# Kernel tuning notes

Measured on AMD Instinct MI355X. Metric: run time of the kernel, lower is better.

Reference implementation:

```python
import jax, jax.numpy as jnp
import numpy as np

B, S, E, H, HD, M = 2, 2048, 1024, 16, 64, 2048  # batch, seq, embed, heads, head_dim, mem_width


def setup_inputs() -> dict:
    key = jax.random.key(0)
    k1, k2, k3, k4, k5 = jax.random.split(key, 5)
    tensor = jax.random.normal(k1, (B, S, E), dtype=jnp.float32)
    # QueryProj: Linear(E -> [H, HD]) with weight + bias (kaiming-style scale)
    Wq = jax.random.normal(k2, (E, H, HD), dtype=jnp.float32) / np.sqrt(E)
    bq = jnp.zeros((H, HD), dtype=jnp.float32)
    # Learnable key/value memory banks [H, M, HD]
    K = jax.random.normal(k3, (H, M, HD), dtype=jnp.float32) / np.sqrt(HD)
    V = jax.random.normal(k4, (H, M, HD), dtype=jnp.float32) / np.sqrt(HD)
    # DeheadProj: Linear([H, HD] -> E)
    Wd = jax.random.normal(k5, (H, HD, E), dtype=jnp.float32) / np.sqrt(H * HD)
    bd = jnp.zeros((E,), dtype=jnp.float32)
    return {"tensor": tensor, "Wq": Wq, "bq": bq, "K": K, "V": V, "Wd": Wd, "bd": bd}


def reference(tensor, Wq, bq, K, V, Wd, bd):
    # Head-splitting query projection: [B,S,E] -> [B,S,H,HD]
    q = jnp.einsum('bse,ehd->bshd', tensor, Wq) + bq
    # Attention logits against fixed parameter memory: [B,S,H,M]
    logits = jnp.einsum('bshd,hmd->bshm', q, K)
    score = jax.nn.softmax(logits, axis=-1)  # mode == 'softmax'
    # Value readout, scaled AFTER the matmul by sqrt(head_dim) (as in source)
    attn = jnp.einsum('bshm,hmd->bshd', score, V) / jnp.sqrt(jnp.asarray(HD, dtype=q.dtype))
    # Dehead projection back to embedding width: [B,S,E]
    out = jnp.einsum('bshd,hde->bse', attn, Wd) + bd
    return out
```

## Files before the change

kernel.cpp:

```cpp
#include <hip/hip_runtime.h>

typedef _Float16 half8 __attribute__((ext_vector_type(8)));
typedef _Float16 half4v __attribute__((ext_vector_type(4)));
typedef __fp16 fp16x2 __attribute__((ext_vector_type(2)));
typedef float f32x4 __attribute__((ext_vector_type(4)));
typedef float float4v __attribute__((ext_vector_type(4)));

constexpr int NS = 4096;
constexpr int E  = 1024;
constexpr int H  = 16;
constexpr int HD = 64;
constexpr int M  = 2048;
constexpr int HE = 1024;

__device__ __forceinline__ void gload16(const _Float16* g, _Float16* l) {
  __builtin_amdgcn_global_load_lds((__attribute__((address_space(1))) void*)g,
                                   (__attribute__((address_space(3))) void*)l, 16, 0, 0);
}

__device__ __forceinline__ float fexp2(float x) {
#if __has_builtin(__builtin_amdgcn_exp2f)
  return __builtin_amdgcn_exp2f(x);
#else
  return __expf(x * 0.6931471805599453f);
#endif
}


__global__ void cvt_f32_to_f16(const float* __restrict__ in, _Float16* __restrict__ out,
                               float scale) {
  int i = (blockIdx.x * 256 + threadIdx.x) * 4;
  float4v v = *(const float4v*)(in + i);
  half4v o = { (_Float16)(v[0] * scale), (_Float16)(v[1] * scale),
               (_Float16)(v[2] * scale), (_Float16)(v[3] * scale) };
  *(half4v*)(out + i) = o;
}

__global__ void transpose_cvt(const float* __restrict__ in, _Float16* __restrict__ out,
                              int R, int C) {
  __shared__ float tile[32][33];
  int b = blockIdx.z;
  in  += (size_t)b * R * C;
  out += (size_t)b * R * C;
  int c0 = blockIdx.x * 32, r0 = blockIdx.y * 32;
  int tx = threadIdx.x, ty = threadIdx.y;
#pragma unroll
  for (int i = 0; i < 4; ++i)
    tile[ty + 8 * i][tx] = in[(size_t)(r0 + ty + 8 * i) * C + c0 + tx];
  __syncthreads();
#pragma unroll
  for (int i = 0; i < 4; ++i)
    out[(size_t)(c0 + ty + 8 * i) * R + r0 + tx] = (_Float16)tile[tx][ty + 8 * i];
}

__global__ void transpose_cvt2(const float* __restrict__ inA, const float* __restrict__ inB,
                               _Float16* __restrict__ outA, _Float16* __restrict__ outB) {
  __shared__ float tile[32][33];
  const float* in = blockIdx.z ? inB : inA;
  _Float16* out = blockIdx.z ? outB : outA;
  int c0 = blockIdx.x * 32, r0 = blockIdx.y * 32;
  int tx = threadIdx.x, ty = threadIdx.y;
#pragma unroll
  for (int i = 0; i < 4; ++i)
    tile[ty + 8 * i][tx] = in[(size_t)(r0 + ty + 8 * i) * 1024 + c0 + tx];
  __syncthreads();
#pragma unroll
  for (int i = 0; i < 4; ++i)
    out[(size_t)(c0 + ty + 8 * i) * 1024 + r0 + tx] = (_Float16)tile[tx][ty + 8 * i];
}


template <typename OUT_T>
__global__ __launch_bounds__(512, 4) void gemm_f16(
    const _Float16* __restrict__ A,
    const _Float16* __restrict__ Bt,
    const float* __restrict__ bias,
    OUT_T* __restrict__ C,
    int Ncols, int K, float scale)
{
  __shared__ alignas(16) _Float16 Ab[2][8 * 512];
  __shared__ alignas(16) _Float16 Bb[2][4 * 512];
  const int tid = threadIdx.x;
  const int wave = tid >> 6, lane = tid & 63;
  const int l15 = lane & 15, l4 = lane >> 4;

  const int nwg = gridDim.x;
  int wg = (blockIdx.x & 7) * (nwg >> 3) + (blockIdx.x >> 3);
  const int nbn = Ncols >> 6;
  const int mblk = wg / nbn, nblk = wg % nbn;

  const _Float16* aS = A  + (size_t)(mblk * 128 + wave * 16 + l15) * K + l4 * 8;
  const _Float16* bS = Bt + (size_t)(nblk * 64 + (wave & 3) * 16 + l15) * K + l4 * 8;
  _Float16* aD0 = &Ab[0][wave * 512];
  _Float16* aD1 = &Ab[1][wave * 512];
  _Float16* bD0 = &Bb[0][(wave & 3) * 512];
  _Float16* bD1 = &Bb[1][(wave & 3) * 512];

  const int wr = wave >> 1, wc = wave & 1;
  f32x4 acc[2][2];
#pragma unroll
  for (int i = 0; i < 2; ++i)
#pragma unroll
    for (int n = 0; n < 2; ++n) acc[i][n] = (f32x4){0.f, 0.f, 0.f, 0.f};

  gload16(aS, aD0);
  if (wave < 4) gload16(bS, bD0);
  aS += 32; bS += 32;

  const int nk = K >> 5;
  for (int kt = 0; kt < nk; ++kt) {
    if (kt + 1 < nk) {
      gload16(aS, (kt & 1) ? aD0 : aD1);
      if (wave < 4) gload16(bS, (kt & 1) ? bD0 : bD1);
      aS += 32; bS += 32;
      if (wave < 4) { asm volatile("s_waitcnt vmcnt(2)" ::: "memory"); }
      else          { asm volatile("s_waitcnt vmcnt(1)" ::: "memory"); }
    } else {
      asm volatile("s_waitcnt vmcnt(0)" ::: "memory");
    }
    __builtin_amdgcn_s_barrier();
    const _Float16* Ac = (kt & 1) ? &Ab[1][0] : &Ab[0][0];
    const _Float16* Bc = (kt & 1) ? &Bb[1][0] : &Bb[0][0];
    half8 af[2], bf[2];
#pragma unroll
    for (int i = 0; i < 2; ++i) af[i] = *(const half8*)(Ac + (wr * 2 + i) * 512 + lane * 8);
#pragma unroll
    for (int n = 0; n < 2; ++n) bf[n] = *(const half8*)(Bc + (wc * 2 + n) * 512 + lane * 8);
    __builtin_amdgcn_s_setprio(1);
#pragma unroll
    for (int i = 0; i < 2; ++i)
#pragma unroll
      for (int n = 0; n < 2; ++n)
        acc[i][n] = __builtin_amdgcn_mfma_f32_16x16x32_f16(af[i], bf[n], acc[i][n], 0, 0, 0);
    __builtin_amdgcn_s_setprio(0);
    asm volatile("s_waitcnt lgkmcnt(0)" ::: "memory");
    __builtin_amdgcn_sched_barrier(0);
    __builtin_amdgcn_s_barrier();
  }

  const int row0 = mblk * 128 + wr * 32;
  const int col0 = nblk * 64 + wc * 32;
#pragma unroll
  for (int n = 0; n < 2; ++n) {
    int col = col0 + n * 16 + l15;
    float bv = bias[col];
#pragma unroll
    for (int i = 0; i < 2; ++i)
#pragma unroll
      for (int r = 0; r < 4; ++r) {
        int row = row0 + i * 16 + l4 * 4 + r;
        C[(size_t)row * Ncols + col] = (OUT_T)(acc[i][n][r] * scale + bv);
      }
  }
}


__global__ __launch_bounds__(256, 4) void attn_fused(
    const _Float16* __restrict__ qh,
    const _Float16* __restrict__ Kh,
    const _Float16* __restrict__ Vth,
    _Float16* __restrict__ Op0,
    _Float16* __restrict__ Op1,
    float* __restrict__ Spart)
{
  __shared__ alignas(16) _Float16 Kb[2][4096];
  __shared__ alignas(16) _Float16 Vb[2][4096];
  __shared__ alignas(16) _Float16 Pl[4096];

  int wg = (blockIdx.x & 7) * 128 + (blockIdx.x >> 3);
  const int h = wg >> 6, half = (wg >> 5) & 1, sblk = wg & 31;
  const int m0 = half * 1024;
  const int tid = threadIdx.x;
  const int wave = tid >> 6, lane = tid & 63, l15 = lane & 15, l4 = lane >> 4;
  const int s0 = sblk * 128 + wave * 32;

  half8 qf[2][2];
#pragma unroll
  for (int f = 0; f < 2; ++f) {
    const _Float16* qp = qh + (size_t)(s0 + f * 16 + l15) * HE + h * HD + l4 * 8;
    qf[f][0] = *(const half8*)qp;
    qf[f][1] = *(const half8*)(qp + 32);
  }

  const _Float16* kSrc = Kh + (size_t)h * M * HD
                         + (size_t)((wave >> 1) * 16 + l15) * HD + (wave & 1) * 32 + l4 * 8;
  const _Float16* vSrc = Vth + (size_t)h * HD * M + (size_t)(wave * 16 + l15) * M + l4 * 8;
  const int dOff = wave * 512 + lane * 8;

  _Float16* Pw = &Pl[wave * 1024];
  const int pAddr = (l4 >> 1) * 128 + l15 * 8 + (l4 & 1) * 4;

  half8 vones;
#pragma unroll
  for (int j = 0; j < 8; ++j) vones[j] = (_Float16)1.0f;

  f32x4 acc[2][4];
  f32x4 accs[2];
#pragma unroll
  for (int f = 0; f < 2; ++f) {
    accs[f] = (f32x4){0.f, 0.f, 0.f, 0.f};
#pragma unroll
    for (int n = 0; n < 4; ++n) acc[f][n] = (f32x4){0.f, 0.f, 0.f, 0.f};
  }

#define STAGE(b, mm) {                                          \
    gload16(kSrc + (size_t)(mm) * HD,        &Kb[b][dOff]);     \
    gload16(kSrc + (size_t)((mm) + 32) * HD, &Kb[b][dOff + 2048]); \
    gload16(vSrc + (mm),                     &Vb[b][dOff]);     \
    gload16(vSrc + (mm) + 32,                &Vb[b][dOff + 2048]); }

#define CHALF(b, hh) {                                                                     \
    const _Float16* Kc = &Kb[b][(hh) * 2048];                                              \
    const _Float16* Vc = &Vb[b][(hh) * 2048];                                              \
    half8 kf[4], vf[4];                                                                    \
    _Pragma("unroll")                                                                      \
    for (int c = 0; c < 4; ++c) {                                                          \
      kf[c] = *(const half8*)(Kc + c * 512 + lane * 8);                                    \
      vf[c] = *(const half8*)(Vc + c * 512 + lane * 8);                                    \
    }                                                                                      \
    f32x4 z = (f32x4){0.f, 0.f, 0.f, 0.f};                                                 \
    f32x4 s[2][2];                                                                         \
    __builtin_amdgcn_s_setprio(1);                                                         \
    _Pragma("unroll")                                                                      \
    for (int f = 0; f < 2; ++f)                                                            \
      _Pragma("unroll")                                                                    \
      for (int t = 0; t < 2; ++t) {                                                        \
        s[f][t] = __builtin_amdgcn_mfma_f32_16x16x32_f16(kf[t * 2 + 0], qf[f][0], z, 0, 0, 0); \
        s[f][t] = __builtin_amdgcn_mfma_f32_16x16x32_f16(kf[t * 2 + 1], qf[f][1], s[f][t], 0, 0, 0); \
      }                                                                                    \
    __builtin_amdgcn_s_setprio(0);                                                         \
    _Pragma("unroll")                                                                      \
    for (int f = 0; f < 2; ++f)                                                            \
      _Pragma("unroll")                                                                    \
      for (int t = 0; t < 2; ++t) {                                                        \
        fp16x2 lo = __builtin_amdgcn_cvt_pkrtz(fexp2(s[f][t][0]), fexp2(s[f][t][1]));      \
        fp16x2 hi = __builtin_amdgcn_cvt_pkrtz(fexp2(s[f][t][2]), fexp2(s[f][t][3]));      \
        *(fp16x2*)(Pw + pAddr + f * 512 + t * 256)     = lo;                               \
        *(fp16x2*)(Pw + pAddr + f * 512 + t * 256 + 2) = hi;                               \
      }                                                                                    \
    asm volatile("s_waitcnt lgkmcnt(0)" ::: "memory");                                     \
    __builtin_amdgcn_sched_barrier(0);                                                     \
    half8 pf0 = *(const half8*)(Pw + lane * 8);                                            \
    half8 pf1 = *(const half8*)(Pw + 512 + lane * 8);                                      \
    __builtin_amdgcn_s_setprio(1);                                                         \
    _Pragma("unroll")                                                                      \
    for (int n = 0; n < 4; ++n) {                                                          \
      acc[0][n] = __builtin_amdgcn_mfma_f32_16x16x32_f16(pf0, vf[n], acc[0][n], 0, 0, 0);  \
      acc[1][n] = __builtin_amdgcn_mfma_f32_16x16x32_f16(pf1, vf[n], acc[1][n], 0, 0, 0);  \
    }                                                                                      \
    accs[0] = __builtin_amdgcn_mfma_f32_16x16x32_f16(pf0, vones, accs[0], 0, 0, 0);        \
    accs[1] = __builtin_amdgcn_mfma_f32_16x16x32_f16(pf1, vones, accs[1], 0, 0, 0);        \
    __builtin_amdgcn_s_setprio(0);                                                         \
  }

  STAGE(0, m0);
  for (int kt = 0; kt < 16; ++kt) {
    const int cur = kt & 1;
    if (kt < 15) {
      STAGE(cur ^ 1, m0 + (kt + 1) * 64);
      asm volatile("s_waitcnt vmcnt(4)" ::: "memory");
    } else {
      asm volatile("s_waitcnt vmcnt(0)" ::: "memory");
    }
    __builtin_amdgcn_s_barrier();
    CHALF(cur, 0);
    CHALF(cur, 1);
    __builtin_amdgcn_s_barrier();
  }

  _Float16* Op = half ? Op1 : Op0;
  float* Sp = Spart + (size_t)half * (NS * H);
#pragma unroll
  for (int f = 0; f < 2; ++f) {
#pragma unroll
    for (int n = 0; n < 4; ++n)
#pragma unroll
      for (int r = 0; r < 4; ++r) {
        int row = s0 + f * 16 + l4 * 4 + r;
        Op[(size_t)row * HE + h * HD + n * 16 + l15] = (_Float16)acc[f][n][r];
      }
    if (l15 == 0) {
#pragma unroll
      for (int r = 0; r < 4; ++r) {
        int row = s0 + f * 16 + l4 * 4 + r;
        Sp[(size_t)row * H + h] = accs[f][r];
      }
    }
  }
#undef STAGE
#undef CHALF
}

__global__ void attn_combine(const _Float16* __restrict__ O0, const _Float16* __restrict__ O1,
                             const float* __restrict__ Spart, _Float16* __restrict__ out) {
  int idx = (blockIdx.x * 256 + threadIdx.x) * 8;
  int row = idx >> 10, he = idx & 1023, h = he >> 6;
  half8 a = *(const half8*)(O0 + idx);
  half8 b = *(const half8*)(O1 + idx);
  float s = Spart[(size_t)row * H + h] + Spart[(size_t)(NS + row) * H + h];
  float inv = 1.0f / s;
  half8 o;
#pragma unroll
  for (int j = 0; j < 8; ++j) o[j] = (_Float16)(((float)a[j] + (float)b[j]) * inv);
  *(half8*)(out + idx) = o;
}


extern "C" void kernel_launch(void* const* d_in, const int* in_sizes, int n_in,
                              void* d_out, int out_size, void* d_ws, size_t ws_size,
                              hipStream_t stream) {
  const float* tensor = (const float*)d_in[0];
  const float* Wq     = (const float*)d_in[1];
  const float* bq     = (const float*)d_in[2];
  const float* Kp     = (const float*)d_in[3];
  const float* Vp     = (const float*)d_in[4];
  const float* Wd     = (const float*)d_in[5];
  const float* bd     = (const float*)d_in[6];
  float* out = (float*)d_out;

  char* ws = (char*)d_ws;
  _Float16* th    = (_Float16*)(ws);
  _Float16* qhb   = (_Float16*)(ws + (8  << 20));
  _Float16* attnh = (_Float16*)(ws + (16 << 20));
  _Float16* Wqt   = (_Float16*)(ws + (24 << 20));
  _Float16* Wdt   = (_Float16*)(ws + (26 << 20));
  _Float16* Khb   = (_Float16*)(ws + (28 << 20));
  _Float16* Vth   = (_Float16*)(ws + (32 << 20));
  _Float16* Op0   = (_Float16*)(ws);
  _Float16* Op1   = (_Float16*)(ws + (36 << 20));
  float*    Spart = (float*)(ws + (24 << 20));

  cvt_f32_to_f16<<<(NS * E) / 1024, 256, 0, stream>>>(tensor, th, 1.0f);
  cvt_f32_to_f16<<<(H * M * HD) / 1024, 256, 0, stream>>>(Kp, Khb, 1.44269504088896f);
  transpose_cvt2<<<dim3(32, 32, 2), dim3(32, 8), 0, stream>>>(Wq, Wd, Wqt, Wdt);
  transpose_cvt<<<dim3(2, 64, 16), dim3(32, 8), 0, stream>>>(Vp, Vth, 2048, 64);

  gemm_f16<_Float16><<<512, 512, 0, stream>>>(th, Wqt, bq, qhb, HE, E, 1.0f);
  attn_fused<<<1024, 256, 0, stream>>>(qhb, Khb, Vth, Op0, Op1, Spart);
  attn_combine<<<(NS * HE) / 2048, 256, 0, stream>>>(Op0, Op1, Spart, attnh);
  gemm_f16<float><<<512, 512, 0, stream>>>(attnh, Wdt, bd, out, E, HE, 0.125f);
}
```

Before: 120.9 us.

## Software-pipeline PV matmul one tile behind QK and exp in attention loop

After: 130.2 us. 7.6% more time.

```diff
diff --git a/kernel.cpp b/kernel.cpp
--- a/kernel.cpp
+++ b/kernel.cpp
@@ -155,7 +155,7 @@
 }
 
 
-__global__ __launch_bounds__(256, 4) void attn_fused(
+__global__ __launch_bounds__(256, 3) void attn_fused(
     const _Float16* __restrict__ qh,
     const _Float16* __restrict__ Kh,
     const _Float16* __restrict__ Vth,
@@ -203,55 +203,66 @@
     for (int n = 0; n < 4; ++n) acc[f][n] = (f32x4){0.f, 0.f, 0.f, 0.f};
   }
 
-#define STAGE(b, mm) {                                          \
-    gload16(kSrc + (size_t)(mm) * HD,        &Kb[b][dOff]);     \
+  half8 pfp[2][2];
+  half8 vfp[2][4];
+  f32x4 s[2][2];
+
+#define STAGE(b, mm) {                                             \
+    gload16(kSrc + (size_t)(mm) * HD,        &Kb[b][dOff]);        \
     gload16(kSrc + (size_t)((mm) + 32) * HD, &Kb[b][dOff + 2048]); \
-    gload16(vSrc + (mm),                     &Vb[b][dOff]);     \
+    gload16(vSrc + (mm),                     &Vb[b][dOff]);        \
     gload16(vSrc + (mm) + 32,                &Vb[b][dOff + 2048]); }
 
-#define CHALF(b, hh) {                                                                     \
-    const _Float16* Kc = &Kb[b][(hh) * 2048];                                              \
-    const _Float16* Vc = &Vb[b][(hh) * 2048];                                              \
-    half8 kf[4], vf[4];                                                                    \
-    _Pragma("unroll")                                                                      \
-    for (int c = 0; c < 4; ++c) {                                                          \
-      kf[c] = *(const half8*)(Kc + c * 512 + lane * 8);                                    \
-      vf[c] = *(const half8*)(Vc + c * 512 + lane * 8);                                    \
-    }                                                                                      \
-    f32x4 z = (f32x4){0.f, 0.f, 0.f, 0.f};                                                 \
-    f32x4 s[2][2];                                                                         \
-    __builtin_amdgcn_s_setprio(1);                                                         \
-    _Pragma("unroll")                                                                      \
-    for (int f = 0; f < 2; ++f)                                                            \
-      _Pragma("unroll")                                                                    \
-      for (int t = 0; t < 2; ++t) {                                                        \
+#define QKH(b, hh) {                                                                      \
+    const _Float16* Kc = &Kb[b][(hh) * 2048];                                             \
+    half8 kf[4];                                                                          \
+    _Pragma("unroll")                                                                     \
+    for (int c = 0; c < 4; ++c) kf[c] = *(const half8*)(Kc + c * 512 + lane * 8);         \
+    f32x4 z = (f32x4){0.f, 0.f, 0.f, 0.f};                                                \
+    __builtin_amdgcn_s_setprio(1);                                                        \
+    _Pragma("unroll")                                                                     \
+    for (int f = 0; f < 2; ++f)                                                           \
+      _Pragma("unroll")                                                                   \
+      for (int t = 0; t < 2; ++t) {                                                       \
         s[f][t] = __builtin_amdgcn_mfma_f32_16x16x32_f16(kf[t * 2 + 0], qf[f][0], z, 0, 0, 0); \
         s[f][t] = __builtin_amdgcn_mfma_f32_16x16x32_f16(kf[t * 2 + 1], qf[f][1], s[f][t], 0, 0, 0); \
-      }                                                                                    \
-    __builtin_amdgcn_s_setprio(0);                                                         \
-    _Pragma("unroll")                                                                      \
-    for (int f = 0; f < 2; ++f)                                                            \
-      _Pragma("unroll")                                                                    \
-      for (int t = 0; t < 2; ++t) {                                                        \
-        fp16x2 lo = __builtin_amdgcn_cvt_pkrtz(fexp2(s[f][t][0]), fexp2(s[f][t][1]));      \
-        fp16x2 hi = __builtin_amdgcn_cvt_pkrtz(fexp2(s[f][t][2]), fexp2(s[f][t][3]));      \
-        *(fp16x2*)(Pw + pAddr + f * 512 + t * 256)     = lo;                               \
-        *(fp16x2*)(Pw + pAddr + f * 512 + t * 256 + 2) = hi;                               \
-      }                                                                                    \
-    asm volatile("s_waitcnt lgkmcnt(0)" ::: "memory");                                     \
-    __builtin_amdgcn_sched_barrier(0);                                                     \
-    half8 pf0 = *(const half8*)(Pw + lane * 8);                                            \
-    half8 pf1 = *(const half8*)(Pw + 512 + lane * 8);                                      \
-    __builtin_amdgcn_s_setprio(1);                                                         \
-    _Pragma("unroll")                                                                      \
-    for (int n = 0; n < 4; ++n) {                                                          \
-      acc[0][n] = __builtin_amdgcn_mfma_f32_16x16x32_f16(pf0, vf[n], acc[0][n], 0, 0, 0);  \
-      acc[1][n] = __builtin_amdgcn_mfma_f32_16x16x32_f16(pf1, vf[n], acc[1][n], 0, 0, 0);  \
-    }                                                                                      \
-    accs[0] = __builtin_amdgcn_mfma_f32_16x16x32_f16(pf0, vones, accs[0], 0, 0, 0);        \
-    accs[1] = __builtin_amdgcn_mfma_f32_16x16x32_f16(pf1, vones, accs[1], 0, 0, 0);        \
-    __builtin_amdgcn_s_setprio(0);                                                         \
-  }
+      }                                                                                   \
+    __builtin_amdgcn_s_setprio(0); }
+
+#define PVH(hh) {                                                                         \
+    __builtin_amdgcn_s_setprio(1);                                                        \
+    _Pragma("unroll")                                                                     \
+    for (int n = 0; n < 4; ++n) {                                                         \
+      acc[0][n] = __builtin_amdgcn_mfma_f32_16x16x32_f16(pfp[hh][0], vfp[hh][n], acc[0][n], 0, 0, 0); \
+      acc[1][n] = __builtin_amdgcn_mfma_f32_16x16x32_f16(pfp[hh][1], vfp[hh][n], acc[1][n], 0, 0, 0); \
+    }                                                                                     \
+    accs[0] = __builtin_amdgcn_mfma_f32_16x16x32_f16(pfp[hh][0], vones, accs[0], 0, 0, 0); \
+    accs[1] = __builtin_amdgcn_mfma_f32_16x16x32_f16(pfp[hh][1], vones, accs[1], 0, 0, 0); \
+    __builtin_amdgcn_s_setprio(0); }
+
+#define EXPW() {                                                                          \
+    _Pragma("unroll")                                                                     \
+    for (int f = 0; f < 2; ++f)                                                           \
+      _Pragma("unroll")                                                                   \
+      for (int t = 0; t < 2; ++t) {                                                       \
+        fp16x2 lo = __builtin_amdgcn_cvt_pkrtz(fexp2(s[f][t][0]), fexp2(s[f][t][1]));     \
+        fp16x2 hi = __builtin_amdgcn_cvt_pkrtz(fexp2(s[f][t][2]), fexp2(s[f][t][3]));     \
+        *(fp16x2*)(Pw + pAddr + f * 512 + t * 256)     = lo;                              \
+        *(fp16x2*)(Pw + pAddr + f * 512 + t * 256 + 2) = hi;                              \
+      } }
+
+#define RDPF(hh) {                                                                        \
+    asm volatile("s_waitcnt lgkmcnt(0)" ::: "memory");                                    \
+    __builtin_amdgcn_sched_barrier(0);                                                    \
+    pfp[hh][0] = *(const half8*)(Pw + lane * 8);                                          \
+    pfp[hh][1] = *(const half8*)(Pw + 512 + lane * 8); }
+
+#define VREAD(b) {                                                                        \
+    _Pragma("unroll")                                                                     \
+    for (int hh = 0; hh < 2; ++hh)                                                        \
+      _Pragma("unroll")                                                                   \
+      for (int c = 0; c < 4; ++c)                                                         \
+        vfp[hh][c] = *(const half8*)(&Vb[b][(hh) * 2048] + c * 512 + lane * 8); }
 
   STAGE(0, m0);
   for (int kt = 0; kt < 16; ++kt) {
@@ -263,10 +274,19 @@
       asm volatile("s_waitcnt vmcnt(0)" ::: "memory");
     }
     __builtin_amdgcn_s_barrier();
-    CHALF(cur, 0);
-    CHALF(cur, 1);
+    QKH(cur, 0);
+    if (kt) PVH(0);
+    EXPW();
+    RDPF(0);
+    QKH(cur, 1);
+    if (kt) PVH(1);
+    VREAD(cur);
+    EXPW();
+    RDPF(1);
     __builtin_amdgcn_s_barrier();
   }
+  PVH(0);
+  PVH(1);
 
   _Float16* Op = half ? Op1 : Op0;
   float* Sp = Spart + (size_t)half * (NS * H);
@@ -288,7 +308,11 @@
     }
   }
 #undef STAGE
-#undef CHALF
+#undef QKH
+#undef PVH
+#undef EXPW
+#undef RDPF
+#undef VREAD
 }
 
 __global__ void attn_combine(const _Float16* __restrict__ O0, const _Float16* __restrict__ O1,
```

## Switch attention to 32x32 MFMA with register-resident P via permlane32 swap

Applied to the files above, without the earlier changes.

Result: slower. 126.9 us (+5.0%).

```diff
diff --git a/kernel.cpp b/kernel.cpp
--- a/kernel.cpp
+++ b/kernel.cpp
@@ -4,7 +4,9 @@
 typedef _Float16 half4v __attribute__((ext_vector_type(4)));
 typedef __fp16 fp16x2 __attribute__((ext_vector_type(2)));
 typedef float f32x4 __attribute__((ext_vector_type(4)));
+typedef float f32x16 __attribute__((ext_vector_type(16)));
 typedef float float4v __attribute__((ext_vector_type(4)));
+typedef unsigned uint32x2 __attribute__((ext_vector_type(2)));
 
 constexpr int NS = 4096;
 constexpr int E  = 1024;
@@ -24,6 +26,30 @@
 #else
   return __expf(x * 0.6931471805599453f);
 #endif
+}
+
+__device__ __forceinline__ unsigned pkh(float a, float b) {
+  fp16x2 t = __builtin_amdgcn_cvt_pkrtz(a, b);
+  return __builtin_bit_cast(unsigned, t);
+}
+
+__device__ __forceinline__ uint32x2 pl32swap(unsigned a, unsigned b) {
+#if __has_builtin(__builtin_amdgcn_permlane32_swap)
+  return __builtin_amdgcn_permlane32_swap(a, b, false, false);
+#else
+  unsigned sa = (unsigned)__shfl_xor((int)a, 32, 64);
+  unsigned sb = (unsigned)__shfl_xor((int)b, 32, 64);
+  uint32x2 r;
+  r.x = (threadIdx.x & 32) ? sb : a;
+  r.y = (threadIdx.x & 32) ? b : sa;
+  return r;
+#endif
+}
+
+__device__ __forceinline__ half8 mk8(unsigned a, unsigned b, unsigned c, unsigned d) {
+  union { unsigned u[4]; half8 h; } t;
+  t.u[0] = a; t.u[1] = b; t.u[2] = c; t.u[3] = d;
+  return t.h;
 }
 
 
@@ -165,93 +191,39 @@
 {
   __shared__ alignas(16) _Float16 Kb[2][4096];
   __shared__ alignas(16) _Float16 Vb[2][4096];
-  __shared__ alignas(16) _Float16 Pl[4096];
 
   int wg = (blockIdx.x & 7) * 128 + (blockIdx.x >> 3);
   const int h = wg >> 6, half = (wg >> 5) & 1, sblk = wg & 31;
   const int m0 = half * 1024;
   const int tid = threadIdx.x;
-  const int wave = tid >> 6, lane = tid & 63, l15 = lane & 15, l4 = lane >> 4;
+  const int wave = tid >> 6, lane = tid & 63;
+  const int l31 = lane & 31, hi = lane >> 5;
   const int s0 = sblk * 128 + wave * 32;
 
-  half8 qf[2][2];
-#pragma unroll
-  for (int f = 0; f < 2; ++f) {
-    const _Float16* qp = qh + (size_t)(s0 + f * 16 + l15) * HE + h * HD + l4 * 8;
-    qf[f][0] = *(const half8*)qp;
-    qf[f][1] = *(const half8*)(qp + 32);
-  }
-
-  const _Float16* kSrc = Kh + (size_t)h * M * HD
-                         + (size_t)((wave >> 1) * 16 + l15) * HD + (wave & 1) * 32 + l4 * 8;
-  const _Float16* vSrc = Vth + (size_t)h * HD * M + (size_t)(wave * 16 + l15) * M + l4 * 8;
-  const int dOff = wave * 512 + lane * 8;
-
-  _Float16* Pw = &Pl[wave * 1024];
-  const int pAddr = (l4 >> 1) * 128 + l15 * 8 + (l4 & 1) * 4;
-
-  half8 vones;
-#pragma unroll
-  for (int j = 0; j < 8; ++j) vones[j] = (_Float16)1.0f;
-
-  f32x4 acc[2][4];
-  f32x4 accs[2];
-#pragma unroll
-  for (int f = 0; f < 2; ++f) {
-    accs[f] = (f32x4){0.f, 0.f, 0.f, 0.f};
-#pragma unroll
-    for (int n = 0; n < 4; ++n) acc[f][n] = (f32x4){0.f, 0.f, 0.f, 0.f};
-  }
-
-#define STAGE(b, mm) {                                          \
-    gload16(kSrc + (size_t)(mm) * HD,        &Kb[b][dOff]);     \
-    gload16(kSrc + (size_t)((mm) + 32) * HD, &Kb[b][dOff + 2048]); \
-    gload16(vSrc + (mm),                     &Vb[b][dOff]);     \
-    gload16(vSrc + (mm) + 32,                &Vb[b][dOff + 2048]); }
-
-#define CHALF(b, hh) {                                                                     \
-    const _Float16* Kc = &Kb[b][(hh) * 2048];                                              \
-    const _Float16* Vc = &Vb[b][(hh) * 2048];                                              \
-    half8 kf[4], vf[4];                                                                    \
-    _Pragma("unroll")                                                                      \
-    for (int c = 0; c < 4; ++c) {                                                          \
-      kf[c] = *(const half8*)(Kc + c * 512 + lane * 8);                                    \
-      vf[c] = *(const half8*)(Vc + c * 512 + lane * 8);                                    \
-    }                                                                                      \
-    f32x4 z = (f32x4){0.f, 0.f, 0.f, 0.f};                                                 \
-    f32x4 s[2][2];                                                                         \
-    __builtin_amdgcn_s_setprio(1);                                                         \
-    _Pragma("unroll")                                                                      \
-    for (int f = 0; f < 2; ++f)                                                            \
-      _Pragma("unroll")                                                                    \
-      for (int t = 0; t < 2; ++t) {                                                        \
-        s[f][t] = __builtin_amdgcn_mfma_f32_16x16x32_f16(kf[t * 2 + 0], qf[f][0], z, 0, 0, 0); \
-        s[f][t] = __builtin_amdgcn_mfma_f32_16x16x32_f16(kf[t * 2 + 1], qf[f][1], s[f][t], 0, 0, 0); \
-      }                                                                                    \
-    __builtin_amdgcn_s_setprio(0);                                                         \
-    _Pragma("unroll")                                                                      \
-    for (int f = 0; f < 2; ++f)                                                            \
-      _Pragma("unroll")                                                                    \
-      for (int t = 0; t < 2; ++t) {                                                        \
-        fp16x2 lo = __builtin_amdgcn_cvt_pkrtz(fexp2(s[f][t][0]), fexp2(s[f][t][1]));      \
-        fp16x2 hi = __builtin_amdgcn_cvt_pkrtz(fexp2(s[f][t][2]), fexp2(s[f][t][3]));      \
-        *(fp16x2*)(Pw + pAddr + f * 512 + t * 256)     = lo;                               \
-        *(fp16x2*)(Pw + pAddr + f * 512 + t * 256 + 2) = hi;                               \
-      }                                                                                    \
-    asm volatile("s_waitcnt lgkmcnt(0)" ::: "memory");                                     \
-    __builtin_amdgcn_sched_barrier(0);                                                     \
-    half8 pf0 = *(const half8*)(Pw + lane * 8);                                            \
-    half8 pf1 = *(const half8*)(Pw + 512 + lane * 8);                                      \
-    __builtin_amdgcn_s_setprio(1);                                                         \
-    _Pragma("unroll")                                                                      \
-    for (int n = 0; n < 4; ++n) {                                                          \
-      acc[0][n] = __builtin_amdgcn_mfma_f32_16x16x32_f16(pf0, vf[n], acc[0][n], 0, 0, 0);  \
-      acc[1][n] = __builtin_amdgcn_mfma_f32_16x16x32_f16(pf1, vf[n], acc[1][n], 0, 0, 0);  \
-    }                                                                                      \
-    accs[0] = __builtin_amdgcn_mfma_f32_16x16x32_f16(pf0, vones, accs[0], 0, 0, 0);        \
-    accs[1] = __builtin_amdgcn_mfma_f32_16x16x32_f16(pf1, vones, accs[1], 0, 0, 0);        \
-    __builtin_amdgcn_s_setprio(0);                                                         \
-  }
+  half8 qf[4];
+  {
+    const _Float16* qp = qh + (size_t)(s0 + l31) * HE + h * HD + hi * 8;
+    qf[0] = *(const half8*)(qp);
+    qf[1] = *(const half8*)(qp + 16);
+    qf[2] = *(const half8*)(qp + 32);
+    qf[3] = *(const half8*)(qp + 48);
+  }
+
+  const _Float16* kS = Kh + (size_t)h * M * HD
+                       + (size_t)((wave >> 1) * 32 + l31) * HD + (wave & 1) * 32 + hi * 8;
+  const _Float16* vS = Vth + (size_t)(h * HD + (wave & 1) * 32 + l31) * M
+                       + (wave >> 1) * 32 + hi * 8;
+  const int dOff = wave * 1024 + lane * 8;
+
+  f32x16 accA = {0.f,0.f,0.f,0.f,0.f,0.f,0.f,0.f,0.f,0.f,0.f,0.f,0.f,0.f,0.f,0.f};
+  f32x16 accB = {0.f,0.f,0.f,0.f,0.f,0.f,0.f,0.f,0.f,0.f,0.f,0.f,0.f,0.f,0.f,0.f};
+  float lsum = 0.f;
+
+#define STAGE(b, mm) {                                        \
+    gload16(kS + (size_t)(mm) * HD,      &Kb[b][dOff]);       \
+    gload16(kS + (size_t)(mm) * HD + 16, &Kb[b][dOff + 512]); \
+    gload16(vS + (mm),                   &Vb[b][dOff]);       \
+    gload16(vS + (mm) + 16,              &Vb[b][dOff + 512]); }
 
   STAGE(0, m0);
   for (int kt = 0; kt < 16; ++kt) {
@@ -263,32 +235,64 @@
       asm volatile("s_waitcnt vmcnt(0)" ::: "memory");
     }
     __builtin_amdgcn_s_barrier();
-    CHALF(cur, 0);
-    CHALF(cur, 1);
+
+#pragma unroll
+    for (int mt = 0; mt < 2; ++mt) {
+      const _Float16* Kc = &Kb[cur][mt * 2048];
+      const _Float16* Vc = &Vb[cur][mt * 2048];
+      half8 kf0 = *(const half8*)(Kc + lane * 8);
+      half8 kf1 = *(const half8*)(Kc + 512 + lane * 8);
+      half8 kf2 = *(const half8*)(Kc + 1024 + lane * 8);
+      half8 kf3 = *(const half8*)(Kc + 1536 + lane * 8);
+      f32x16 s = {0.f,0.f,0.f,0.f,0.f,0.f,0.f,0.f,0.f,0.f,0.f,0.f,0.f,0.f,0.f,0.f};
+      __builtin_amdgcn_s_setprio(1);
+      s = __builtin_amdgcn_mfma_f32_32x32x16_f16(kf0, qf[0], s, 0, 0, 0);
+      s = __builtin_amdgcn_mfma_f32_32x32x16_f16(kf1, qf[1], s, 0, 0, 0);
+      s = __builtin_amdgcn_mfma_f32_32x32x16_f16(kf2, qf[2], s, 0, 0, 0);
+      s = __builtin_amdgcn_mfma_f32_32x32x16_f16(kf3, qf[3], s, 0, 0, 0);
+      __builtin_amdgcn_s_setprio(0);
+      unsigned pd[8];
+      float la = 0.f;
+#pragma unroll
+      for (int i = 0; i < 8; ++i) {
+        float a = fexp2(s[2 * i]);
+        float b = fexp2(s[2 * i + 1]);
+        la += a + b;
+        pd[i] = pkh(a, b);
+      }
+      lsum += la;
+      uint32x2 w0 = pl32swap(pd[0], pd[2]);
+      uint32x2 w1 = pl32swap(pd[1], pd[3]);
+      uint32x2 w2 = pl32swap(pd[4], pd[6]);
+      uint32x2 w3 = pl32swap(pd[5], pd[7]);
+      half8 pa0 = mk8(w0.x, w1.x, w0.y, w1.y);
+      half8 pa1 = mk8(w2.x, w3.x, w2.y, w3.y);
+      half8 v00 = *(const half8*)(Vc + lane * 8);
+      half8 v01 = *(const half8*)(Vc + 512 + lane * 8);
+      half8 v10 = *(const half8*)(Vc + 1024 + lane * 8);
+      half8 v11 = *(const half8*)(Vc + 1536 + lane * 8);
+      __builtin_amdgcn_s_setprio(1);
+      accA = __builtin_amdgcn_mfma_f32_32x32x16_f16(pa0, v00, accA, 0, 0, 0);
+      accA = __builtin_amdgcn_mfma_f32_32x32x16_f16(pa1, v01, accA, 0, 0, 0);
+      accB = __builtin_amdgcn_mfma_f32_32x32x16_f16(pa0, v10, accB, 0, 0, 0);
+      accB = __builtin_amdgcn_mfma_f32_32x32x16_f16(pa1, v11, accB, 0, 0, 0);
+      __builtin_amdgcn_s_setprio(0);
+    }
+    asm volatile("s_waitcnt lgkmcnt(0)" ::: "memory");
     __builtin_amdgcn_s_barrier();
   }
+#undef STAGE
 
   _Float16* Op = half ? Op1 : Op0;
   float* Sp = Spart + (size_t)half * (NS * H);
 #pragma unroll
-  for (int f = 0; f < 2; ++f) {
-#pragma unroll
-    for (int n = 0; n < 4; ++n)
-#pragma unroll
-      for (int r = 0; r < 4; ++r) {
-        int row = s0 + f * 16 + l4 * 4 + r;
-        Op[(size_t)row * HE + h * HD + n * 16 + l15] = (_Float16)acc[f][n][r];
-      }
-    if (l15 == 0) {
-#pragma unroll
-      for (int r = 0; r < 4; ++r) {
-        int row = s0 + f * 16 + l4 * 4 + r;
-        Sp[(size_t)row * H + h] = accs[f][r];
-      }
-    }
-  }
-#undef STAGE
-#undef CHALF
+  for (int r = 0; r < 16; ++r) {
+    int q = s0 + (r & 3) + 8 * (r >> 2) + 4 * hi;
+    Op[(size_t)q * HE + h * HD + l31]      = (_Float16)accA[r];
+    Op[(size_t)q * HE + h * HD + 32 + l31] = (_Float16)accB[r];
+  }
+  float tot = lsum + __shfl_xor(lsum, 32, 64);
+  if (hi == 0) Sp[(size_t)(s0 + l31) * H + h] = tot;
 }
 
 __global__ void attn_combine(const _Float16* __restrict__ O0, const _Float16* __restrict__ O1,
```
